# Kernel tuning notes

Hardware: AMD Instinct MI355X
Metric: run time of the kernel (lower is better)

The kernel has to match this reference:

```python
import jax, jax.numpy as jnp
import numpy as np

LAYERS = 2          # init kwarg 'layers'
DEPTH = 4           # init kwarg 'depth' (StronglyEntanglingLayers depth)
N_QUBITS = 4
MULT = float(np.pi - np.finfo(np.float32).eps)


def _apply_1q(state, U, q):
    """state: (B,2,2,2,2) complex; U: (2,2) or (B,2,2) complex; wire q (axis 1+q, MSB-first)."""
    st = jnp.moveaxis(state, 1 + q, -1)
    if U.ndim == 3:
        st = jnp.einsum('bij,b...j->b...i', U, st)
    else:
        st = jnp.einsum('ij,...j->...i', U, st)
    return jnp.moveaxis(st, -1, 1 + q)


def _apply_cnot(state, c, t):
    st = jnp.moveaxis(state, (1 + c, 1 + t), (-2, -1))
    st = jnp.stack([st[..., 0, :], st[..., 1, ::-1]], axis=-2)
    return jnp.moveaxis(st, (-2, -1), (1 + c, 1 + t))


def _ry(theta):
    """RY(theta) -> (...,2,2) complex64; theta may be batched."""
    c = jnp.cos(theta / 2).astype(jnp.complex64)
    s = jnp.sin(theta / 2).astype(jnp.complex64)
    return jnp.stack([jnp.stack([c, -s], -1), jnp.stack([s, c], -1)], -2)


def _rot(phi, theta, omega):
    """qml.Rot = RZ(omega) RY(theta) RZ(phi), scalar params -> (2,2) complex64."""
    c = jnp.cos(theta / 2)
    s = jnp.sin(theta / 2)
    ep = jnp.exp(-0.5j * (phi + omega).astype(jnp.complex64))
    em = jnp.exp(0.5j * (phi - omega).astype(jnp.complex64))
    row0 = jnp.stack([ep * c, -em * s])
    row1 = jnp.stack([jnp.conj(em) * s, jnp.conj(ep) * c])
    return jnp.stack([row0, row1])


def _circuit(x, w, n_out):
    """AngleEmbedding(Y) + StronglyEntanglingLayers on 4 qubits.
    x: (B,4) angles; w: (L,4,3); returns (B, n_out) PauliZ expvals."""
    B = x.shape[0]
    state = jnp.zeros((B, 16), jnp.complex64).at[:, 0].set(1.0).reshape(B, 2, 2, 2, 2)
    for q in range(N_QUBITS):
        state = _apply_1q(state, _ry(x[:, q]), q)  # batched RY embedding
    L = w.shape[0]
    for l in range(L):
        for q in range(N_QUBITS):
            state = _apply_1q(state, _rot(w[l, q, 0], w[l, q, 1], w[l, q, 2]), q)
        r = (l % (N_QUBITS - 1)) + 1  # default SEL ranges: 1,2,3,1,...
        for q in range(N_QUBITS):
            state = _apply_cnot(state, q, (q + r) % N_QUBITS)
    probs = state.real ** 2 + state.imag ** 2  # (B,2,2,2,2)
    outs = []
    for q in range(n_out):
        axes = tuple(a for a in range(1, 5) if a != 1 + q)
        pq = probs.sum(axes)  # (B,2)
        outs.append(pq[:, 0] - pq[:, 1])
    return jnp.stack(outs, axis=1)


def _forward(x_, theta):
    B = x_.shape[0]
    z = jnp.zeros((B, 1), x_.dtype)
    H = jnp.concatenate([z, x_, z, z], axis=1)  # (B,16)
    c44 = jax.vmap(lambda xb, wb: _circuit(xb, wb, 4))  # over 4 blocks
    c41 = jax.vmap(lambda xb, wb: _circuit(xb, wb, 1))
    # layer 0: 'first' -> contiguous 4-wide blocks
    blocks = H.reshape(B, 4, 4).transpose(1, 0, 2)  # (block, B, 4)
    H = c44(blocks, theta[0]).transpose(1, 0, 2).reshape(B, 16)
    # hidden layers: 'multiple' -> block j = column j of each old block
    for i in range(LAYERS):
        blocks = H.reshape(B, 4, 4).transpose(2, 0, 1)  # (j, B, old_block)
        H = c44(blocks, theta[i + 3]).transpose(1, 0, 2).reshape(B, 16)
    # 16 -> 4 : 'multiple' transpose, 4to1 readout per block
    blocks = H.reshape(B, 4, 4).transpose(2, 0, 1)
    H = c41(blocks, theta[1]).transpose(1, 0, 2).reshape(B, 4)
    # 4 -> 1 : single block, only theta[2][0] is used (matches original loop)
    H = _circuit(H, theta[2, 0], 1)  # (B,1)
    return (H * MULT).astype(jnp.float32)


def setup_inputs() -> dict:
    key = jax.random.key(0)
    k1, k2 = jax.random.split(key)
    x_ = jax.random.uniform(k1, (32768, 13), dtype=jnp.float32)
    theta = 0.01 * jax.random.normal(k2, (LAYERS + 3, 4, DEPTH, 4, 3), dtype=jnp.float32)
    return {"x_": x_, "theta": theta}


def reference(x_, theta):
    return _forward(x_, theta)
```

## Files before the change

### kernel.cpp

```cpp
#include <hip/hip_runtime.h>
#include <math.h>


typedef _Float16 half8 __attribute__((ext_vector_type(8)));
typedef float floatx16 __attribute__((ext_vector_type(16)));

#define N_CIRC 17
__device__ __constant__ constexpr int PERM[3][16] = {
  {0, 9, 11, 2, 15, 6, 4, 13, 7, 14, 12, 5, 8, 1, 3, 10},
  {0, 5, 10, 15, 1, 4, 11, 14, 2, 7, 8, 13, 3, 6, 9, 12},
  {0, 3, 6, 5, 12, 15, 10, 9, 11, 8, 13, 14, 7, 4, 1, 2},
};

__global__ void __launch_bounds__(64) build_M_kernel(
    const float* __restrict__ theta, _Float16* __restrict__ M) {
  int idx = blockIdx.x * 64 + threadIdx.x;
  if (idx >= N_CIRC * 16) return;
  int c = idx >> 4, j = idx & 15;
  int tt, blk;
  if (c < 4)       { tt = 0; blk = c; }
  else if (c < 8)  { tt = 3; blk = c - 4; }
  else if (c < 12) { tt = 4; blk = c - 8; }
  else if (c < 16) { tt = 1; blk = c - 12; }
  else             { tt = 2; blk = 0; }
  float sr[16], si[16];
#pragma unroll
  for (int i = 0; i < 16; ++i) { sr[i] = 0.f; si[i] = 0.f; }
  sr[j] = 1.f;
#pragma unroll
  for (int l = 0; l < 4; ++l) {
#pragma unroll
    for (int q = 0; q < 4; ++q) {
      const float* th = theta + (((tt * 4 + blk) * 16) + l * 4 + q) * 3;
      float phi = th[0], the = th[1], ome = th[2];
      float st, ct;   __sincosf(0.5f * the, &st, &ct);
      float sap, cap; __sincosf(0.5f * (phi + ome), &sap, &cap);
      float sam, cam; __sincosf(0.5f * (phi - ome), &sam, &cam);
      float u00r =  cap * ct, u00i = -sap * ct;
      float u01r = -cam * st, u01i = -sam * st;
      float u10r =  cam * st, u10i = -sam * st;
      float u11r =  cap * ct, u11i =  sap * ct;
      const int m = 8 >> q;
#pragma unroll
      for (int i = 0; i < 16; ++i) {
        if (i & m) continue;
        const int i1 = i | m;
        float ar = sr[i], ai = si[i], br = sr[i1], bi = si[i1];
        sr[i]  = u00r * ar - u00i * ai + u01r * br - u01i * bi;
        si[i]  = u00r * ai + u00i * ar + u01r * bi + u01i * br;
        sr[i1] = u10r * ar - u10i * ai + u11r * br - u11i * bi;
        si[i1] = u10r * ai + u10i * ar + u11r * bi + u11i * br;
      }
    }
    const int ri = (l == 3) ? 0 : l;
    float tr[16], ti[16];
#pragma unroll
    for (int i = 0; i < 16; ++i) { tr[i] = sr[i]; ti[i] = si[i]; }
#pragma unroll
    for (int i = 0; i < 16; ++i) { sr[PERM[ri][i]] = tr[i]; si[PERM[ri][i]] = ti[i]; }
  }
#pragma unroll
  for (int m = 0; m < 32; ++m) {
    float val = (m & 1) ? si[m >> 1] : sr[m >> 1];
    int lane = ((j >> 3) << 5) | m;
    M[(size_t)(c * 64 + lane) * 8 + (j & 7)] = (_Float16)val;
  }
}

__global__ void __launch_bounds__(256, 4) vqc_kernel(
    const float* __restrict__ x, const _Float16* __restrict__ M,
    float* __restrict__ out, int B) {
  __shared__ float Hb[2][16][32];

  const int tid  = threadIdx.x;
  const int w    = tid >> 6;
  const int lane = tid & 63;
  const int g = lane >> 5, n = lane & 31;
  const int row_base = blockIdx.x * 32;

  for (int i = tid; i < 32 * 13; i += 256) {
    int r = i / 13, j = i - 13 * r;
    Hb[0][1 + j][r] = (row_base + r < B) ? x[(row_base + r) * 13 + j] : 0.f;
  }
  if (tid < 32) { Hb[0][0][tid] = 0.f; Hb[0][14][tid] = 0.f; Hb[0][15][tid] = 0.f; }
  __syncthreads();

  float e_final = 0.f;

#pragma unroll
  for (int s = 0; s < 5; ++s) {
    const int rb = s & 1, wb = rb ^ 1;
    const bool active = (s < 4) || (w == 0);
    const int ci = (s < 4) ? (s * 4 + w) : 16;
    float x0, x1, x2, x3;
    if (s == 0) {
      x0 = Hb[rb][4 * w + 0][n]; x1 = Hb[rb][4 * w + 1][n];
      x2 = Hb[rb][4 * w + 2][n]; x3 = Hb[rb][4 * w + 3][n];
    } else if (s < 4) {
      x0 = Hb[rb][w][n];      x1 = Hb[rb][4 + w][n];
      x2 = Hb[rb][8 + w][n];  x3 = Hb[rb][12 + w][n];
    } else {
      x0 = Hb[rb][0][n]; x1 = Hb[rb][1][n];
      x2 = Hb[rb][2][n]; x3 = Hb[rb][3][n];
    }

    float le0 = 0.f, le1 = 0.f, le2 = 0.f, le3 = 0.f;
    if (active) {
      float s0, c0, s1, c1, s2, c2, s3, c3;
      __sincosf(0.5f * x0, &s0, &c0);
      __sincosf(0.5f * x1, &s1, &c1);
      __sincosf(0.5f * x2, &s2, &c2);
      __sincosf(0.5f * x3, &s3, &c3);
      float w0 = g ? s0 : c0;
      float u0 = w0 * c1, u1 = w0 * s1;
      float w23[4] = {c2 * c3, c2 * s3, s2 * c3, s2 * s3};
      half8 bf;
#pragma unroll
      for (int t = 0; t < 8; ++t)
        bf[t] = (_Float16)(((t < 4) ? u0 : u1) * w23[t & 3]);
      half8 a = *(const half8*)&M[(size_t)(ci * 64 + lane) * 8];
      floatx16 z = {0.f,0.f,0.f,0.f,0.f,0.f,0.f,0.f,
                    0.f,0.f,0.f,0.f,0.f,0.f,0.f,0.f};
      floatx16 acc = __builtin_amdgcn_mfma_f32_32x32x16_f16(a, bf, z, 0, 0, 0);
      float p[4][2];
#pragma unroll
      for (int qq = 0; qq < 4; ++qq)
#pragma unroll
        for (int h = 0; h < 2; ++h)
          p[qq][h] = acc[4 * qq + 2 * h]     * acc[4 * qq + 2 * h]
                   + acc[4 * qq + 2 * h + 1] * acc[4 * qq + 2 * h + 1];
      float S4[4], D4[4];
#pragma unroll
      for (int qq = 0; qq < 4; ++qq) {
        S4[qq] = p[qq][0] + p[qq][1];
        D4[qq] = p[qq][0] - p[qq][1];
      }
      le0 = (S4[0] + S4[1]) - (S4[2] + S4[3]);
      le0 += __shfl_xor(le0, 32);
      if (s < 3) {
        le1 = (S4[0] - S4[1]) + (S4[2] - S4[3]);
        float S = (S4[0] + S4[1]) + (S4[2] + S4[3]);
        le2 = g ? -S : S;
        le3 = (D4[0] + D4[1]) + (D4[2] + D4[3]);
        le1 += __shfl_xor(le1, 32);
        le2 += __shfl_xor(le2, 32);
        le3 += __shfl_xor(le3, 32);
      }
    }
    if (s < 3) {
      if (g == 0) {
        Hb[wb][4 * w + 0][n] = le0; Hb[wb][4 * w + 1][n] = le1;
        Hb[wb][4 * w + 2][n] = le2; Hb[wb][4 * w + 3][n] = le3;
      }
    } else if (s == 3) {
      if (g == 0) Hb[wb][w][n] = le0;
    } else {
      e_final = le0;
    }
    __syncthreads();
  }

  if (w == 0 && g == 0 && row_base + n < B) {
    const float MULT = (float)(3.141592653589793 - 1.1920928955078125e-07);
    out[row_base + n] = e_final * MULT;
  }
}

extern "C" void kernel_launch(void* const* d_in, const int* in_sizes, int n_in,
                              void* d_out, int out_size, void* d_ws, size_t ws_size,
                              hipStream_t stream) {
  const float* x     = (const float*)d_in[0];
  const float* theta = (const float*)d_in[1];
  float* out = (float*)d_out;
  _Float16* M = (_Float16*)d_ws;
  int B = in_sizes[0] / 13;
  hipLaunchKernelGGL(build_M_kernel, dim3((N_CIRC * 16 + 63) / 64), dim3(64),
                     0, stream, theta, M);
  int blocks = (B + 31) / 32;
  hipLaunchKernelGGL(vqc_kernel, dim3(blocks), dim3(256), 0, stream,
                     x, M, out, B);
}
```

Measured before the change: 64.47 us.

## Fuse unitary-matrix build into main kernel and process 64 rows per block

```diff
diff --git a/kernel.cpp b/kernel.cpp
--- a/kernel.cpp
+++ b/kernel.cpp
@@ -12,77 +12,78 @@
   {0, 3, 6, 5, 12, 15, 10, 9, 11, 8, 13, 14, 7, 4, 1, 2},
 };
 
-__global__ void __launch_bounds__(64) build_M_kernel(
-    const float* __restrict__ theta, _Float16* __restrict__ M) {
-  int idx = blockIdx.x * 64 + threadIdx.x;
-  if (idx >= N_CIRC * 16) return;
-  int c = idx >> 4, j = idx & 15;
-  int tt, blk;
-  if (c < 4)       { tt = 0; blk = c; }
-  else if (c < 8)  { tt = 3; blk = c - 4; }
-  else if (c < 12) { tt = 4; blk = c - 8; }
-  else if (c < 16) { tt = 1; blk = c - 12; }
-  else             { tt = 2; blk = 0; }
-  float sr[16], si[16];
-#pragma unroll
-  for (int i = 0; i < 16; ++i) { sr[i] = 0.f; si[i] = 0.f; }
-  sr[j] = 1.f;
-#pragma unroll
-  for (int l = 0; l < 4; ++l) {
-#pragma unroll
-    for (int q = 0; q < 4; ++q) {
-      const float* th = theta + (((tt * 4 + blk) * 16) + l * 4 + q) * 3;
-      float phi = th[0], the = th[1], ome = th[2];
-      float st, ct;   __sincosf(0.5f * the, &st, &ct);
-      float sap, cap; __sincosf(0.5f * (phi + ome), &sap, &cap);
-      float sam, cam; __sincosf(0.5f * (phi - ome), &sam, &cam);
-      float u00r =  cap * ct, u00i = -sap * ct;
-      float u01r = -cam * st, u01i = -sam * st;
-      float u10r =  cam * st, u10i = -sam * st;
-      float u11r =  cap * ct, u11i =  sap * ct;
-      const int m = 8 >> q;
-#pragma unroll
-      for (int i = 0; i < 16; ++i) {
-        if (i & m) continue;
-        const int i1 = i | m;
-        float ar = sr[i], ai = si[i], br = sr[i1], bi = si[i1];
-        sr[i]  = u00r * ar - u00i * ai + u01r * br - u01i * bi;
-        si[i]  = u00r * ai + u00i * ar + u01r * bi + u01i * br;
-        sr[i1] = u10r * ar - u10i * ai + u11r * br - u11i * bi;
-        si[i1] = u10r * ai + u10i * ar + u11r * bi + u11i * br;
-      }
-    }
-    const int ri = (l == 3) ? 0 : l;
-    float tr[16], ti[16];
-#pragma unroll
-    for (int i = 0; i < 16; ++i) { tr[i] = sr[i]; ti[i] = si[i]; }
-#pragma unroll
-    for (int i = 0; i < 16; ++i) { sr[PERM[ri][i]] = tr[i]; si[PERM[ri][i]] = ti[i]; }
-  }
-#pragma unroll
-  for (int m = 0; m < 32; ++m) {
-    float val = (m & 1) ? si[m >> 1] : sr[m >> 1];
-    int lane = ((j >> 3) << 5) | m;
-    M[(size_t)(c * 64 + lane) * 8 + (j & 7)] = (_Float16)val;
-  }
-}
-
-__global__ void __launch_bounds__(256, 4) vqc_kernel(
-    const float* __restrict__ x, const _Float16* __restrict__ M,
+__global__ void __launch_bounds__(512, 4) vqc_fused_kernel(
+    const float* __restrict__ x, const float* __restrict__ theta,
     float* __restrict__ out, int B) {
-  __shared__ float Hb[2][16][32];
+  __shared__ _Float16 Mlds[N_CIRC * 64 * 8] __attribute__((aligned(16)));
+  __shared__ float Hb[2][16][64];
 
   const int tid  = threadIdx.x;
-  const int w    = tid >> 6;
+  const int w8   = tid >> 6;
+  const int rg   = w8 >> 2;
+  const int w    = w8 & 3;
   const int lane = tid & 63;
   const int g = lane >> 5, n = lane & 31;
-  const int row_base = blockIdx.x * 32;
+  const int nn = rg * 32 + n;
+  const int row_base = blockIdx.x * 64;
 
-  for (int i = tid; i < 32 * 13; i += 256) {
+  for (int i = tid; i < 64 * 13; i += 512) {
     int r = i / 13, j = i - 13 * r;
     Hb[0][1 + j][r] = (row_base + r < B) ? x[(row_base + r) * 13 + j] : 0.f;
   }
-  if (tid < 32) { Hb[0][0][tid] = 0.f; Hb[0][14][tid] = 0.f; Hb[0][15][tid] = 0.f; }
+  if (tid < 64) { Hb[0][0][tid] = 0.f; Hb[0][14][tid] = 0.f; Hb[0][15][tid] = 0.f; }
+
+  if (tid < N_CIRC * 16) {
+    const int c = tid >> 4, j = tid & 15;
+    int tt, blk;
+    if (c < 4)       { tt = 0; blk = c; }
+    else if (c < 8)  { tt = 3; blk = c - 4; }
+    else if (c < 12) { tt = 4; blk = c - 8; }
+    else if (c < 16) { tt = 1; blk = c - 12; }
+    else             { tt = 2; blk = 0; }
+    float sr[16], si[16];
+#pragma unroll
+    for (int i = 0; i < 16; ++i) { sr[i] = 0.f; si[i] = 0.f; }
+    sr[j] = 1.f;
+#pragma unroll
+    for (int l = 0; l < 4; ++l) {
+#pragma unroll
+      for (int q = 0; q < 4; ++q) {
+        const float* th = theta + (((tt * 4 + blk) * 16) + l * 4 + q) * 3;
+        float phi = th[0], the = th[1], ome = th[2];
+        float st, ct;   __sincosf(0.5f * the, &st, &ct);
+        float sap, cap; __sincosf(0.5f * (phi + ome), &sap, &cap);
+        float sam, cam; __sincosf(0.5f * (phi - ome), &sam, &cam);
+        float u00r =  cap * ct, u00i = -sap * ct;
+        float u01r = -cam * st, u01i = -sam * st;
+        float u10r =  cam * st, u10i = -sam * st;
+        float u11r =  cap * ct, u11i =  sap * ct;
+        const int m = 8 >> q;
+#pragma unroll
+        for (int i = 0; i < 16; ++i) {
+          if (i & m) continue;
+          const int i1 = i | m;
+          float ar = sr[i], ai = si[i], br = sr[i1], bi = si[i1];
+          sr[i]  = u00r * ar - u00i * ai + u01r * br - u01i * bi;
+          si[i]  = u00r * ai + u00i * ar + u01r * bi + u01i * br;
+          sr[i1] = u10r * ar - u10i * ai + u11r * br - u11i * bi;
+          si[i1] = u10r * ai + u10i * ar + u11r * bi + u11i * br;
+        }
+      }
+      const int ri = (l == 3) ? 0 : l;
+      float tr[16], ti[16];
+#pragma unroll
+      for (int i = 0; i < 16; ++i) { tr[i] = sr[i]; ti[i] = si[i]; }
+#pragma unroll
+      for (int i = 0; i < 16; ++i) { sr[PERM[ri][i]] = tr[i]; si[PERM[ri][i]] = ti[i]; }
+    }
+#pragma unroll
+    for (int m = 0; m < 32; ++m) {
+      float val = (m & 1) ? si[m >> 1] : sr[m >> 1];
+      int ln = ((j >> 3) << 5) | m;
+      Mlds[(c * 64 + ln) * 8 + (j & 7)] = (_Float16)val;
+    }
+  }
   __syncthreads();
 
   float e_final = 0.f;
@@ -94,18 +95,19 @@
     const int ci = (s < 4) ? (s * 4 + w) : 16;
     float x0, x1, x2, x3;
     if (s == 0) {
-      x0 = Hb[rb][4 * w + 0][n]; x1 = Hb[rb][4 * w + 1][n];
-      x2 = Hb[rb][4 * w + 2][n]; x3 = Hb[rb][4 * w + 3][n];
+      x0 = Hb[rb][4 * w + 0][nn]; x1 = Hb[rb][4 * w + 1][nn];
+      x2 = Hb[rb][4 * w + 2][nn]; x3 = Hb[rb][4 * w + 3][nn];
     } else if (s < 4) {
-      x0 = Hb[rb][w][n];      x1 = Hb[rb][4 + w][n];
-      x2 = Hb[rb][8 + w][n];  x3 = Hb[rb][12 + w][n];
+      x0 = Hb[rb][w][nn];      x1 = Hb[rb][4 + w][nn];
+      x2 = Hb[rb][8 + w][nn];  x3 = Hb[rb][12 + w][nn];
     } else {
-      x0 = Hb[rb][0][n]; x1 = Hb[rb][1][n];
-      x2 = Hb[rb][2][n]; x3 = Hb[rb][3][n];
+      x0 = Hb[rb][0][nn]; x1 = Hb[rb][1][nn];
+      x2 = Hb[rb][2][nn]; x3 = Hb[rb][3][nn];
     }
 
     float le0 = 0.f, le1 = 0.f, le2 = 0.f, le3 = 0.f;
     if (active) {
+      half8 a = *(const half8*)&Mlds[(ci * 64 + lane) * 8];
       float s0, c0, s1, c1, s2, c2, s3, c3;
       __sincosf(0.5f * x0, &s0, &c0);
       __sincosf(0.5f * x1, &s1, &c1);
@@ -118,7 +120,6 @@
 #pragma unroll
       for (int t = 0; t < 8; ++t)
         bf[t] = (_Float16)(((t < 4) ? u0 : u1) * w23[t & 3]);
-      half8 a = *(const half8*)&M[(size_t)(ci * 64 + lane) * 8];
       floatx16 z = {0.f,0.f,0.f,0.f,0.f,0.f,0.f,0.f,
                     0.f,0.f,0.f,0.f,0.f,0.f,0.f,0.f};
       floatx16 acc = __builtin_amdgcn_mfma_f32_32x32x16_f16(a, bf, z, 0, 0, 0);
@@ -149,20 +150,20 @@
     }
     if (s < 3) {
       if (g == 0) {
-        Hb[wb][4 * w + 0][n] = le0; Hb[wb][4 * w + 1][n] = le1;
-        Hb[wb][4 * w + 2][n] = le2; Hb[wb][4 * w + 3][n] = le3;
+        Hb[wb][4 * w + 0][nn] = le0; Hb[wb][4 * w + 1][nn] = le1;
+        Hb[wb][4 * w + 2][nn] = le2; Hb[wb][4 * w + 3][nn] = le3;
       }
     } else if (s == 3) {
-      if (g == 0) Hb[wb][w][n] = le0;
+      if (g == 0) Hb[wb][w][nn] = le0;
     } else {
       e_final = le0;
     }
     __syncthreads();
   }
 
-  if (w == 0 && g == 0 && row_base + n < B) {
+  if (w == 0 && g == 0 && row_base + nn < B) {
     const float MULT = (float)(3.141592653589793 - 1.1920928955078125e-07);
-    out[row_base + n] = e_final * MULT;
+    out[row_base + nn] = e_final * MULT;
   }
 }
 
@@ -172,11 +173,8 @@
   const float* x     = (const float*)d_in[0];
   const float* theta = (const float*)d_in[1];
   float* out = (float*)d_out;
-  _Float16* M = (_Float16*)d_ws;
   int B = in_sizes[0] / 13;
-  hipLaunchKernelGGL(build_M_kernel, dim3((N_CIRC * 16 + 63) / 64), dim3(64),
-                     0, stream, theta, M);
-  int blocks = (B + 31) / 32;
-  hipLaunchKernelGGL(vqc_kernel, dim3(blocks), dim3(256), 0, stream,
-                     x, M, out, B);
+  int blocks = (B + 63) / 64;
+  hipLaunchKernelGGL(vqc_fused_kernel, dim3(blocks), dim3(512), 0, stream,
+                     x, theta, out, B);
 }
```

Measured after the change: 77.80 us. +20.7%, slower.

## Run all circuit stages in one wavefront using registers instead of shared memory

Applied to the files above, without the earlier changes.

```diff
diff --git a/kernel.cpp b/kernel.cpp
--- a/kernel.cpp
+++ b/kernel.cpp
@@ -67,102 +67,101 @@
   }
 }
 
-__global__ void __launch_bounds__(256, 4) vqc_kernel(
+__device__ __forceinline__ void run_circ(
+    const _Float16* __restrict__ M, int ci, int lane, int g,
+    float a0, float a1, float a2, float a3, bool full,
+    float& o0, float& o1, float& o2, float& o3) {
+  float s0, c0, s1, c1, s2, c2, s3, c3;
+  __sincosf(0.5f * a0, &s0, &c0);
+  __sincosf(0.5f * a1, &s1, &c1);
+  __sincosf(0.5f * a2, &s2, &c2);
+  __sincosf(0.5f * a3, &s3, &c3);
+  float w0 = g ? s0 : c0;
+  float u0 = w0 * c1, u1 = w0 * s1;
+  float w23[4] = {c2 * c3, c2 * s3, s2 * c3, s2 * s3};
+  half8 bf;
+#pragma unroll
+  for (int t = 0; t < 8; ++t)
+    bf[t] = (_Float16)(((t < 4) ? u0 : u1) * w23[t & 3]);
+  half8 a = *(const half8*)&M[(size_t)(ci * 64 + lane) * 8];
+  floatx16 z = {0.f,0.f,0.f,0.f,0.f,0.f,0.f,0.f,
+                0.f,0.f,0.f,0.f,0.f,0.f,0.f,0.f};
+  floatx16 acc = __builtin_amdgcn_mfma_f32_32x32x16_f16(a, bf, z, 0, 0, 0);
+  float p[4][2];
+#pragma unroll
+  for (int qq = 0; qq < 4; ++qq)
+#pragma unroll
+    for (int h = 0; h < 2; ++h)
+      p[qq][h] = acc[4 * qq + 2 * h]     * acc[4 * qq + 2 * h]
+               + acc[4 * qq + 2 * h + 1] * acc[4 * qq + 2 * h + 1];
+  float S4[4], D4[4];
+#pragma unroll
+  for (int qq = 0; qq < 4; ++qq) {
+    S4[qq] = p[qq][0] + p[qq][1];
+    D4[qq] = p[qq][0] - p[qq][1];
+  }
+  o0 = (S4[0] + S4[1]) - (S4[2] + S4[3]);
+  o0 += __shfl_xor(o0, 32);
+  if (full) {
+    o1 = (S4[0] - S4[1]) + (S4[2] - S4[3]);
+    float S = (S4[0] + S4[1]) + (S4[2] + S4[3]);
+    o2 = g ? -S : S;
+    o3 = (D4[0] + D4[1]) + (D4[2] + D4[3]);
+    o1 += __shfl_xor(o1, 32);
+    o2 += __shfl_xor(o2, 32);
+    o3 += __shfl_xor(o3, 32);
+  }
+}
+
+__global__ void __launch_bounds__(64) vqc_reg_kernel(
     const float* __restrict__ x, const _Float16* __restrict__ M,
     float* __restrict__ out, int B) {
-  __shared__ float Hb[2][16][32];
+  const int lane = threadIdx.x;
+  const int g = lane >> 5, n = lane & 31;
+  const int row = blockIdx.x * 32 + n;
 
-  const int tid  = threadIdx.x;
-  const int w    = tid >> 6;
-  const int lane = tid & 63;
-  const int g = lane >> 5, n = lane & 31;
-  const int row_base = blockIdx.x * 32;
+  float xv[13];
+  const float* xp = x + (size_t)(row < B ? row : 0) * 13;
+#pragma unroll
+  for (int j = 0; j < 13; ++j) xv[j] = xp[j];
 
-  for (int i = tid; i < 32 * 13; i += 256) {
-    int r = i / 13, j = i - 13 * r;
-    Hb[0][1 + j][r] = (row_base + r < B) ? x[(row_base + r) * 13 + j] : 0.f;
-  }
-  if (tid < 32) { Hb[0][0][tid] = 0.f; Hb[0][14][tid] = 0.f; Hb[0][15][tid] = 0.f; }
-  __syncthreads();
+  float e[4][4];
+  float d0 = 0.f, d1 = 0.f, d2 = 0.f;
 
-  float e_final = 0.f;
+  run_circ(M, 0, lane, g, 0.f,    xv[0],  xv[1],  xv[2],  true,
+           e[0][0], e[0][1], e[0][2], e[0][3]);
+  run_circ(M, 1, lane, g, xv[3],  xv[4],  xv[5],  xv[6],  true,
+           e[1][0], e[1][1], e[1][2], e[1][3]);
+  run_circ(M, 2, lane, g, xv[7],  xv[8],  xv[9],  xv[10], true,
+           e[2][0], e[2][1], e[2][2], e[2][3]);
+  run_circ(M, 3, lane, g, xv[11], xv[12], 0.f,    0.f,    true,
+           e[3][0], e[3][1], e[3][2], e[3][3]);
 
 #pragma unroll
-  for (int s = 0; s < 5; ++s) {
-    const int rb = s & 1, wb = rb ^ 1;
-    const bool active = (s < 4) || (w == 0);
-    const int ci = (s < 4) ? (s * 4 + w) : 16;
-    float x0, x1, x2, x3;
-    if (s == 0) {
-      x0 = Hb[rb][4 * w + 0][n]; x1 = Hb[rb][4 * w + 1][n];
-      x2 = Hb[rb][4 * w + 2][n]; x3 = Hb[rb][4 * w + 3][n];
-    } else if (s < 4) {
-      x0 = Hb[rb][w][n];      x1 = Hb[rb][4 + w][n];
-      x2 = Hb[rb][8 + w][n];  x3 = Hb[rb][12 + w][n];
-    } else {
-      x0 = Hb[rb][0][n]; x1 = Hb[rb][1][n];
-      x2 = Hb[rb][2][n]; x3 = Hb[rb][3][n];
-    }
-
-    float le0 = 0.f, le1 = 0.f, le2 = 0.f, le3 = 0.f;
-    if (active) {
-      float s0, c0, s1, c1, s2, c2, s3, c3;
-      __sincosf(0.5f * x0, &s0, &c0);
-      __sincosf(0.5f * x1, &s1, &c1);
-      __sincosf(0.5f * x2, &s2, &c2);
-      __sincosf(0.5f * x3, &s3, &c3);
-      float w0 = g ? s0 : c0;
-      float u0 = w0 * c1, u1 = w0 * s1;
-      float w23[4] = {c2 * c3, c2 * s3, s2 * c3, s2 * s3};
-      half8 bf;
+  for (int s = 1; s <= 2; ++s) {
+    float ne[4][4];
 #pragma unroll
-      for (int t = 0; t < 8; ++t)
-        bf[t] = (_Float16)(((t < 4) ? u0 : u1) * w23[t & 3]);
-      half8 a = *(const half8*)&M[(size_t)(ci * 64 + lane) * 8];
-      floatx16 z = {0.f,0.f,0.f,0.f,0.f,0.f,0.f,0.f,
-                    0.f,0.f,0.f,0.f,0.f,0.f,0.f,0.f};
-      floatx16 acc = __builtin_amdgcn_mfma_f32_32x32x16_f16(a, bf, z, 0, 0, 0);
-      float p[4][2];
+    for (int w = 0; w < 4; ++w)
+      run_circ(M, s * 4 + w, lane, g, e[0][w], e[1][w], e[2][w], e[3][w],
+               true, ne[w][0], ne[w][1], ne[w][2], ne[w][3]);
 #pragma unroll
-      for (int qq = 0; qq < 4; ++qq)
+    for (int w = 0; w < 4; ++w)
 #pragma unroll
-        for (int h = 0; h < 2; ++h)
-          p[qq][h] = acc[4 * qq + 2 * h]     * acc[4 * qq + 2 * h]
-                   + acc[4 * qq + 2 * h + 1] * acc[4 * qq + 2 * h + 1];
-      float S4[4], D4[4];
-#pragma unroll
-      for (int qq = 0; qq < 4; ++qq) {
-        S4[qq] = p[qq][0] + p[qq][1];
-        D4[qq] = p[qq][0] - p[qq][1];
-      }
-      le0 = (S4[0] + S4[1]) - (S4[2] + S4[3]);
-      le0 += __shfl_xor(le0, 32);
-      if (s < 3) {
-        le1 = (S4[0] - S4[1]) + (S4[2] - S4[3]);
-        float S = (S4[0] + S4[1]) + (S4[2] + S4[3]);
-        le2 = g ? -S : S;
-        le3 = (D4[0] + D4[1]) + (D4[2] + D4[3]);
-        le1 += __shfl_xor(le1, 32);
-        le2 += __shfl_xor(le2, 32);
-        le3 += __shfl_xor(le3, 32);
-      }
-    }
-    if (s < 3) {
-      if (g == 0) {
-        Hb[wb][4 * w + 0][n] = le0; Hb[wb][4 * w + 1][n] = le1;
-        Hb[wb][4 * w + 2][n] = le2; Hb[wb][4 * w + 3][n] = le3;
-      }
-    } else if (s == 3) {
-      if (g == 0) Hb[wb][w][n] = le0;
-    } else {
-      e_final = le0;
-    }
-    __syncthreads();
+      for (int j = 0; j < 4; ++j) e[w][j] = ne[w][j];
   }
 
-  if (w == 0 && g == 0 && row_base + n < B) {
+  float f[4];
+#pragma unroll
+  for (int w = 0; w < 4; ++w)
+    run_circ(M, 12 + w, lane, g, e[0][w], e[1][w], e[2][w], e[3][w],
+             false, f[w], d0, d1, d2);
+
+  float r;
+  run_circ(M, 16, lane, g, f[0], f[1], f[2], f[3], false, r, d0, d1, d2);
+
+  if (g == 0 && row < B) {
     const float MULT = (float)(3.141592653589793 - 1.1920928955078125e-07);
-    out[row_base + n] = e_final * MULT;
+    out[row] = r * MULT;
   }
 }
 
@@ -177,6 +176,6 @@
   hipLaunchKernelGGL(build_M_kernel, dim3((N_CIRC * 16 + 63) / 64), dim3(64),
                      0, stream, theta, M);
   int blocks = (B + 31) / 32;
-  hipLaunchKernelGGL(vqc_kernel, dim3(blocks), dim3(256), 0, stream,
+  hipLaunchKernelGGL(vqc_reg_kernel, dim3(blocks), dim3(64), 0, stream,
                      x, M, out, B);
 }
```

After: 64.94 us. Within noise of the previous version (+0.7%).
